# Optimization experiments

Hardware: AMD Instinct MI355X
Metric: run time of the kernel (lower is better)

Reference implementation:

```python
import jax, jax.numpy as jnp
import numpy as np
import math

H = 12          # num_attention_heads
DH = 64         # attention_head_size
D = H * DH      # hidden_size = 768
LN_EPS = 1e-5
GAUSS_W = 0.3989422804014327
WIDS = [None, 0.1, 1.0, 5.0]


def gauss_weight(L, wid):
    # faithful to generate_gauss_weight: row-normalized Gaussian bump per query pos
    center = (jnp.arange(L, dtype=jnp.float32) / L)[:, None]       # (L,1)
    pos = jnp.linspace(0.0, 1.0, L, dtype=jnp.float32)[None, :]    # (1,L)
    width = max(wid, 0.01) / 9.0                                   # static python scalar
    g = (GAUSS_W / width) * jnp.exp(-(pos - center) ** 2 / (2.0 * width * width))
    return g / jnp.max(g, axis=-1, keepdims=True)                  # (L,L)


def layer_norm(x, g, b):
    mu = jnp.mean(x, axis=-1, keepdims=True)
    var = jnp.mean((x - mu) ** 2, axis=-1, keepdims=True)
    return (x - mu) * jax.lax.rsqrt(var + LN_EPS) * g + b


def bert_attention(x, mask, qkv_w, qkv_b, out_w, out_b, ln_g, ln_b, wid):
    # x: (N,L,D); mask: (N,L,L); qkv_w: (3,D,D); qkv_b: (3,D)
    N, L, _ = x.shape

    def heads(t):  # (N,L,D) -> (N,H,L,DH)
        return t.reshape(N, L, H, DH).transpose(0, 2, 1, 3)

    q = heads(x @ qkv_w[0] + qkv_b[0])
    k = heads(x @ qkv_w[1] + qkv_b[1])
    v = heads(x @ qkv_w[2] + qkv_b[2])

    scores = jnp.einsum('nhqd,nhkd->nhqk', q, k) / math.sqrt(DH)   # (N,H,L,L)
    if wid is not None:
        scores = scores * gauss_weight(L, wid)[None, None]          # multiplicative GMM mask
    scores = scores + (1.0 - mask[:, None, :, :]) * -10000.0
    probs = jax.nn.softmax(scores, axis=-1)                         # dropout = identity (eval)
    ctx = jnp.einsum('nhqk,nhkd->nhqd', probs, v)                   # (N,H,L,DH)
    ctx = ctx.transpose(0, 2, 1, 3).reshape(N, L, D)

    proj = ctx @ out_w + out_b
    return layer_norm(proj + x, ln_g, ln_b)


def setup_inputs() -> dict:
    key = jax.random.key(0)
    ks = jax.random.split(key, 4)
    N, L = 4, 1024
    s = 0.02
    return {
        'input_tensor': jax.random.normal(ks[0], (N, L, D), dtype=jnp.float32),
        'attention_mask': jnp.ones((N, L, L), dtype=jnp.float32),
        'qkv_w': jax.random.normal(ks[1], (4, 3, D, D), dtype=jnp.float32) * s,
        'qkv_b': jnp.zeros((4, 3, D), dtype=jnp.float32),
        'out_w': jax.random.normal(ks[2], (4, D, D), dtype=jnp.float32) * s,
        'out_b': jnp.zeros((4, D), dtype=jnp.float32),
        'ln_g': jnp.ones((4, D), dtype=jnp.float32),
        'ln_b': jnp.zeros((4, D), dtype=jnp.float32),
    }


def reference(input_tensor, attention_mask, qkv_w, qkv_b, out_w, out_b, ln_g, ln_b):
    # pure_block=False path: 4 parallel GMM-masked attention branches, averaged
    outs = [
        bert_attention(input_tensor, attention_mask,
                       qkv_w[i], qkv_b[i], out_w[i], out_b[i], ln_g[i], ln_b[i], WIDS[i])
        for i in range(4)
    ]
    return jnp.mean(jnp.stack(outs, axis=-1), axis=-1)
```

## Files before the change

### kernel.cpp

```cpp
#include <hip/hip_runtime.h>
#include <hip/hip_bf16.h>

#define NB 4
#define LQ 1024
#define NH 12
#define DHD 64
#define DM 768
#define MTOT (NB*LQ)
#define L2E 1.4426950408889634f
#define SMB 11.541560327111708f
#define CFAR 3.3546262790251185e-4f

typedef __attribute__((ext_vector_type(4))) float f32x4;
typedef __attribute__((ext_vector_type(8))) short bf16x8;
typedef __attribute__((ext_vector_type(4))) short short4v;
typedef unsigned short u16;

#if __has_builtin(__builtin_amdgcn_exp2f)
#define EXP2(x) __builtin_amdgcn_exp2f(x)
#else
#define EXP2(x) __expf((x) * 0.6931471805599453f)
#endif

#define VMCNT(n) asm volatile("s_waitcnt vmcnt(" #n ")" ::: "memory")
#define RAW_BAR() __builtin_amdgcn_s_barrier()

__device__ __forceinline__ u16 f2bf(float f){
  union { float f; unsigned int i; } v; v.f = f;
  unsigned int r = v.i + 0x7FFFu + ((v.i >> 16) & 1u);
  return (u16)(r >> 16);
}
__device__ __forceinline__ float bf2f(u16 u){
  union { unsigned int i; float f; } v; v.i = ((unsigned int)u) << 16;
  return v.f;
}
__device__ __forceinline__ unsigned cvt_pk_bf16(float lo, float hi){
  unsigned r;
  asm("v_cvt_pk_bf16_f32 %0, %1, %2" : "=v"(r) : "v"(lo), "v"(hi));
  return r;
}

typedef const __attribute__((address_space(1))) void* gas_t;
typedef __attribute__((address_space(3))) void* las_t;
__device__ __forceinline__ void gload16(const void* g, void* l){
  __builtin_amdgcn_global_load_lds((gas_t)g, (las_t)l, 16, 0, 0);
}

__global__ void k_cvt_x(const float* __restrict__ x, u16* __restrict__ xb){
  int i = (blockIdx.x * 256 + threadIdx.x) * 4;
  float4 v = *reinterpret_cast<const float4*>(x + i);
  short4v o;
  o[0] = (short)f2bf(v.x); o[1] = (short)f2bf(v.y);
  o[2] = (short)f2bf(v.z); o[3] = (short)f2bf(v.w);
  *reinterpret_cast<short4v*>(xb + i) = o;
}

__global__ void k_wt(const float* __restrict__ qkv_w, const float* __restrict__ out_w,
                     u16* __restrict__ wt){
  int mat = blockIdx.z;
  const float* W = (mat < 12) ? (qkv_w + (size_t)mat*DM*DM)
                              : (out_w + (size_t)(mat-12)*DM*DM);
  __shared__ float tile[32][33];
  int j0 = blockIdx.x*32, k0 = blockIdx.y*32;
  int tx = threadIdx.x, ty = threadIdx.y;
  #pragma unroll
  for (int i=0;i<4;i++)
    tile[ty + i*8][tx] = W[(size_t)(k0 + ty + i*8)*DM + j0 + tx];
  __syncthreads();
  u16* dst = wt + (size_t)mat*DM*DM;
  int tid = ty*32 + tx;
  int jj = tid >> 3, kq = tid & 7;
  short4v pk;
  #pragma unroll
  for (int t=0;t<4;t++) pk[t] = (short)f2bf(tile[kq*4 + t][jj]);
  *reinterpret_cast<short4v*>(&dst[(size_t)(j0 + jj)*DM + k0 + kq*4]) = pk;
}

__global__ void k_maskchk(const float* __restrict__ mask, unsigned* __restrict__ flags){
  int qt = blockIdx.x, kt = blockIdx.y, n = blockIdx.z;
  const float* M = mask + ((size_t)(n*LQ) + qt*64)*LQ + kt*64;
  int tid = threadIdx.x;
  int r = tid >> 2, c4 = (tid & 3) * 16;
  int ok = 1;
  #pragma unroll
  for (int j=0;j<4;j++){
    float4 v = *reinterpret_cast<const float4*>(M + (size_t)r*LQ + c4 + j*4);
    ok &= (v.x==1.f) & (v.y==1.f) & (v.z==1.f) & (v.w==1.f);
  }
  __shared__ int sok[4];
  unsigned long long bal = __ballot(ok);
  if ((tid & 63) == 0) sok[tid>>6] = (bal == 0xFFFFFFFFFFFFFFFFull) ? 1 : 0;
  __syncthreads();
  if (tid == 0) flags[((size_t)n*16 + qt)*16 + kt] = sok[0] & sok[1] & sok[2] & sok[3];
}

__global__ __launch_bounds__(256) void k_vsum(const u16* __restrict__ qkvws, float* __restrict__ ps){
  const int nh = blockIdx.x;
  const int b  = blockIdx.y;
  const size_t blk = (size_t)NB*NH*LQ*DHD;
  const u16* Vt = qkvws + (size_t)(b*3+2)*blk + (size_t)nh*DHD*LQ;
  const int tid = threadIdx.x;
  const int dh = tid >> 2, c = tid & 3;
  float* psb = ps + ((size_t)(b*48 + nh)*17)*64;
  float acc = 0.f;
  for (int kt = 0; kt < 16; ++kt){
    if (c == 0) psb[kt*64 + dh] = acc;
    bf16x8 v0 = *reinterpret_cast<const bf16x8*>(&Vt[(size_t)dh*LQ + kt*64 + c*16]);
    bf16x8 v1 = *reinterpret_cast<const bf16x8*>(&Vt[(size_t)dh*LQ + kt*64 + c*16 + 8]);
    float s = 0.f;
    #pragma unroll
    for (int j=0;j<8;j++) s += bf2f((u16)v0[j]) + bf2f((u16)v1[j]);
    s += __shfl_xor(s, 1);
    s += __shfl_xor(s, 2);
    acc += s;
  }
  if (c == 0) psb[16*64 + dh] = acc;
}

__device__ __forceinline__ void gemm_tile32(const u16* __restrict__ Ag,
                                            const u16* __restrict__ Bg,
                                            u16* smem, f32x4 acc[4][4])
{
  const int tid = threadIdx.x, lane = tid & 63, w = tid >> 6;
  const int wr = (w >> 1) * 64, wc = (w & 1) * 64;
  const int rl = lane & 15, q4 = lane >> 4;
  const int srow = tid >> 2;
  const int su = (tid & 3) ^ ((srow >> 1) & 3);

  #define QSTG(buf, k0_) { \
    _Pragma("unroll") \
    for (int r = 0; r < 2; ++r){ \
      gload16(Ag + (size_t)(r*64 + srow)*DM + (k0_) + su*8, smem + (buf)*8192 + r*2048 + tid*8); \
      gload16(Bg + (size_t)(r*64 + srow)*DM + (k0_) + su*8, smem + (buf)*8192 + 4096 + r*2048 + tid*8); \
    } }

  QSTG(0, 0);
  QSTG(1, 32);
  int cur = 0, nxt2 = 2;
  for (int it = 0; it < 24; ++it){
    if (it + 2 < 24){
      QSTG(nxt2, (it+2)*32);
      VMCNT(8);
    } else if (it + 1 < 24){
      VMCNT(4);
    } else {
      VMCNT(0);
    }
    RAW_BAR();
    __builtin_amdgcn_sched_barrier(0);
    const u16* al = smem + cur*8192;
    const u16* bl = al + 4096;
    bf16x8 af[4], bfr[4];
    #pragma unroll
    for (int f = 0; f < 4; ++f){
      int ra = wr + f*16 + rl, rb = wc + f*16 + rl;
      int ua = q4 ^ ((ra >> 1) & 3), ub = q4 ^ ((rb >> 1) & 3);
      af[f]  = *reinterpret_cast<const bf16x8*>(&al[ra*32 + ua*8]);
      bfr[f] = *reinterpret_cast<const bf16x8*>(&bl[rb*32 + ub*8]);
    }
    #pragma unroll
    for (int mf=0; mf<4; ++mf)
      #pragma unroll
      for (int nf=0; nf<4; ++nf)
        acc[mf][nf] = __builtin_amdgcn_mfma_f32_16x16x32_bf16(af[mf], bfr[nf], acc[mf][nf], 0,0,0);
    RAW_BAR();
    cur = cur + 1 == 3 ? 0 : cur + 1;
    nxt2 = nxt2 + 1 == 3 ? 0 : nxt2 + 1;
  }
  #undef QSTG
}

__global__ __launch_bounds__(256) void k_qkv(const u16* __restrict__ xb, const u16* __restrict__ wt,
                     const float* __restrict__ qkv_b, u16* __restrict__ qkvws)
{
  __shared__ __align__(16) u16 smem[24576];
  const int bid = blockIdx.x;
  const int orig = (bid & 7) * 288 + (bid >> 3);
  const int j0 = (orig % 6) * 128;
  const int m0 = ((orig / 6) % 32) * 128;
  const int mat = orig / 192;
  const int t = mat % 3;
  f32x4 acc[4][4] = {};
  gemm_tile32(xb + (size_t)m0*DM, wt + (size_t)mat*DM*DM + (size_t)j0*DM, smem, acc);

  const int tid = threadIdx.x, lane = tid & 63, w = tid >> 6;
  const int wr = (w >> 1) * 64, wc = (w & 1) * 64;
  const int rl = lane & 15, rg = (lane >> 4) * 4;
  const float sc = (t == 0) ? 0.125f : 1.0f;
  const size_t matbase = (size_t)mat * ((size_t)NB*NH*LQ*DHD);
  if (t < 2){
    #pragma unroll
    for (int nf=0; nf<4; ++nf){
      int jc = wc + nf*16 + rl;
      float bias = qkv_b[mat*DM + j0 + jc];
      #pragma unroll
      for (int mf=0; mf<4; ++mf){
        int row = wr + mf*16 + rg;
        #pragma unroll
        for (int i=0;i<4;i++)
          smem[(row+i)*136 + jc] = f2bf((acc[mf][nf][i] + bias) * sc);
      }
    }
    __syncthreads();
    const int n = m0 >> 10, l0 = m0 & 1023;
    const int hbase = j0 >> 6;
    #pragma unroll
    for (int jj=0; jj<8; ++jj){
      int idx = tid + 256*jj;
      int l = idx >> 4, ch = idx & 15;
      bf16x8 v = *reinterpret_cast<const bf16x8*>(&smem[l*136 + ch*8]);
      int hh = hbase + (ch >> 3);
      int dh0 = (ch & 7) * 8;
      *reinterpret_cast<bf16x8*>(
        &qkvws[matbase + ((size_t)(n*NH + hh)*LQ + l0 + l)*DHD + dh0]) = v;
    }
  } else {
    #pragma unroll
    for (int nf=0; nf<4; ++nf){
      int j = j0 + wc + nf*16 + rl;
      float bias = qkv_b[mat*DM + j];
      int h = j >> 6, dh = j & 63;
      #pragma unroll
      for (int mf=0; mf<4; ++mf){
        int mB = m0 + wr + mf*16 + rg;
        int n = mB >> 10, l = mB & 1023;
        short4v pk;
        #pragma unroll
        for (int i=0;i<4;i++) pk[i] = (short)f2bf(acc[mf][nf][i] + bias);
        *reinterpret_cast<short4v*>(&qkvws[matbase + ((size_t)(n*NH + h)*DHD + dh)*LQ + l]) = pk;
      }
    }
  }
}

__global__ __launch_bounds__(512) void k_attn(const u16* __restrict__ qkvws, const float* __restrict__ mask,
                      const unsigned* __restrict__ flags, const float* __restrict__ ps,
                      u16* __restrict__ ctx, float c2_1, float c2_2, float c2_3)
{
  __shared__ __align__(16) u16 kv_lds[2][2][64*64];
  __shared__ __align__(16) u16 p_lds[128*64];
  const int bid = blockIdx.x;
  const int orig = (bid & 7) * 192 + (bid >> 3);
  const int qp = orig & 7;
  const int b  = (orig >> 3) & 3;
  const int nh = orig >> 5;
  const int n = nh / NH, h = nh % NH;
  const float c2 = (b==1) ? c2_1 : (b==2) ? c2_2 : c2_3;
  const bool useG = (b != 0);
  const int tid = threadIdx.x, lane = tid & 63, w = tid >> 6;
  const int wl = w & 3, half = w >> 2;
  const int qt = qp*2 + half;
  const int rl = lane & 15, q4 = lane >> 4, kc8 = q4*8, rg = q4*4;
  const int q0 = qt*64 + wl*16;

  const size_t hb = (size_t)(n*NH + h);
  const size_t blk = (size_t)NB*NH*LQ*DHD;
  const u16* Qb = qkvws + (size_t)(b*3+0)*blk + hb*LQ*DHD;
  const u16* Kb = qkvws + (size_t)(b*3+1)*blk + hb*LQ*DHD;
  const u16* Vt = qkvws + (size_t)(b*3+2)*blk + hb*DHD*LQ;
  const float* Mb = mask + (size_t)n*LQ*LQ;

  bf16x8 qf0 = *reinterpret_cast<const bf16x8*>(&Qb[(size_t)(q0+rl)*DHD + kc8]);
  bf16x8 qf1 = *reinterpret_cast<const bf16x8*>(&Qb[(size_t)(q0+rl)*DHD + 32 + kc8]);

  float srun[4] = {0.f,0.f,0.f,0.f};
  float dmin2[4], cq[4];
  f32x4 o[4] = {};
  #pragma unroll
  for (int i=0;i<4;i++){
    int q = q0 + rg + i;
    float c = (float)q * (1.0f/1024.0f);
    float ksf = floorf(c * 1023.0f + 0.5f);
    float dm = ksf * (1.0f/1023.0f) - c;
    cq[i] = c; dmin2[i] = dm*dm;
  }

  int lo_a, hi_a, lo_b, hi_b, ra_a, ra_b;
  {
    int qa = qp*2, qb = qp*2+1;
    int r0 = 1, r1 = 1;
    for (int t = 0; t < 16; ++t){
      r0 &= (flags[((size_t)n*16 + qa)*16 + t] != 0u) ? 1 : 0;
      r1 &= (flags[((size_t)n*16 + qb)*16 + t] != 0u) ? 1 : 0;
    }
    ra_a = r0; ra_b = r1;
    lo_a = 0; hi_a = 16; lo_b = 0; hi_b = 16;
    if (r0){
      if (b == 1){ lo_a = qa>0?qa-1:0; hi_a = qa<15?qa+2:16; }
      else if (b == 2){ lo_a = qa>5?qa-5:0; hi_a = qa<10?qa+6:16; }
    }
    if (r1){
      if (b == 1){ lo_b = qb>0?qb-1:0; hi_b = qb<15?qb+2:16; }
      else if (b == 2){ lo_b = qb>5?qb-5:0; hi_b = qb<10?qb+6:16; }
    }
  }
  const int mylo = half ? lo_b : lo_a;
  const int myhi = half ? hi_b : hi_a;
  const int myrowall = half ? ra_b : ra_a;
  const int blo = lo_a < lo_b ? lo_a : lo_b;
  const int bhi = hi_a > hi_b ? hi_a : hi_b;
  const int mynt = myhi - mylo;

  if (myrowall && mynt < 16){
    const float* psb = ps + ((size_t)(b*48 + nh)*17)*64;
    #pragma unroll
    for (int nf=0; nf<4; ++nf){
      int dh = nf*16 + rl;
      float sfar = psb[16*64 + dh] - psb[myhi*64 + dh] + psb[mylo*64 + dh];
      float fv = CFAR * sfar;
      #pragma unroll
      for (int i=0;i<4;i++) o[nf][i] = fv;
    }
    float sinit = CFAR * (float)(64*(16 - mynt));
    #pragma unroll
    for (int i=0;i<4;i++) srun[i] = sinit;
  }

  const int r8 = tid >> 3;
  const int uu = (tid & 7) ^ (r8 & 7);

  #define STAGE8(buf, kt_) { \
    gload16(Kb + (size_t)((kt_)*64 + r8)*DHD + uu*8, (u16*)kv_lds[buf][0] + tid*8); \
    gload16(Vt + (size_t)r8*LQ + (kt_)*64 + uu*8, (u16*)kv_lds[buf][1] + tid*8); }

  STAGE8(0, blo);

  const int nloop = bhi - blo;
  for (int it = 0; it < nloop; ++it){
    const int kt = blo + it;
    const int cur = it & 1;
    if (it + 1 < nloop){
      STAGE8(cur^1, kt+1);
      VMCNT(2);
    } else {
      VMCNT(0);
    }
    RAW_BAR();
    __builtin_amdgcn_sched_barrier(0);

    if (kt >= mylo && kt < myhi){
      const bool allones = myrowall || (flags[((size_t)n*16 + qt)*16 + kt] != 0u);
      const u16* kbuf = (const u16*)kv_lds[cur][0];
      const u16* vbuf = (const u16*)kv_lds[cur][1];

      f32x4 sf[4] = {};
      __builtin_amdgcn_s_setprio(1);
      #pragma unroll
      for (int nf=0; nf<4; ++nf){
        int row = nf*16 + rl, sw = (row & 7) << 3;
        bf16x8 kf0 = *reinterpret_cast<const bf16x8*>(&kbuf[row*64 + (kc8 ^ sw)]);
        bf16x8 kf1 = *reinterpret_cast<const bf16x8*>(&kbuf[row*64 + ((32 + kc8) ^ sw)]);
        sf[nf] = __builtin_amdgcn_mfma_f32_16x16x32_bf16(qf0, kf0, sf[nf], 0,0,0);
        sf[nf] = __builtin_amdgcn_mfma_f32_16x16x32_bf16(qf1, kf1, sf[nf], 0,0,0);
      }
      __builtin_amdgcn_s_setprio(0);

      float pv[4][4];
      #pragma unroll
      for (int nf=0; nf<4; ++nf){
        int key = kt*64 + nf*16 + rl;
        float pos = (float)key * (1.0f/1023.0f);
        #pragma unroll
        for (int i=0;i<4;i++){
          float s = sf[nf][i];
          if (useG){
            float d = pos - cq[i];
            float tg = fmaf(-d, d, dmin2[i]);
            s *= EXP2(tg * c2);
          }
          if (!allones){
            int q = q0 + rg + i;
            s = fmaf(1.0f - Mb[(size_t)q*LQ + key], -10000.0f, s);
          }
          float p = EXP2(fmaf(s, L2E, -SMB));
          srun[i] += p;
          pv[nf][i] = p;
        }
      }

      #pragma unroll
      for (int np=0; np<2; ++np)
        #pragma unroll
        for (int i=0;i<4;i++){
          unsigned u = cvt_pk_bf16(pv[np*2][i], pv[np*2+1][i]);
          int row = w*16 + rg + i, sw = (row & 7) << 3;
          p_lds[row*64 + ((np*32 + rl) ^ sw)]      = (u16)(u & 0xffffu);
          p_lds[row*64 + ((np*32 + 16 + rl) ^ sw)] = (u16)(u >> 16);
        }
      asm volatile("s_waitcnt lgkmcnt(0)" ::: "memory");
      __builtin_amdgcn_sched_barrier(0);

      {
        int prow = w*16 + rl, psw = (prow & 7) << 3;
        bf16x8 pa0 = *reinterpret_cast<const bf16x8*>(&p_lds[prow*64 + (kc8 ^ psw)]);
        bf16x8 pa1 = *reinterpret_cast<const bf16x8*>(&p_lds[prow*64 + ((32 + kc8) ^ psw)]);
        __builtin_amdgcn_s_setprio(1);
        #pragma unroll
        for (int nf=0; nf<4; ++nf){
          int row = nf*16 + rl, sw = (row & 7) << 3;
          bf16x8 vv0 = *reinterpret_cast<const bf16x8*>(&vbuf[row*64 + (kc8 ^ sw)]);
          bf16x8 vv1 = *reinterpret_cast<const bf16x8*>(&vbuf[row*64 + ((32 + kc8) ^ sw)]);
          o[nf] = __builtin_amdgcn_mfma_f32_16x16x32_bf16(pa0, vv0, o[nf], 0,0,0);
          o[nf] = __builtin_amdgcn_mfma_f32_16x16x32_bf16(pa1, vv1, o[nf], 0,0,0);
        }
        __builtin_amdgcn_s_setprio(0);
      }
    }
    RAW_BAR();
  }

  #pragma unroll
  for (int off=1; off<16; off<<=1){
    #pragma unroll
    for (int i=0;i<4;i++) srun[i] += __shfl_xor(srun[i], off);
  }
  #pragma unroll
  for (int i=0;i<4;i++){
    float inv = 1.0f / (srun[i] + 1e-35f);
    int q = q0 + rg + i;
    size_t mrow = ((size_t)(n*LQ + q)) * DM;
    #pragma unroll
    for (int nf=0; nf<4; ++nf){
      int d = h*DHD + nf*16 + rl;
      ctx[(size_t)b*((size_t)MTOT*DM) + mrow + d] = f2bf(o[nf][i] * inv);
    }
  }
  #undef STAGE8
}

__global__ __launch_bounds__(256) void k_proj(const u16* __restrict__ ctx, const u16* __restrict__ wt,
                      const float* __restrict__ out_b, u16* __restrict__ proj)
{
  __shared__ __align__(16) u16 smem[24576];
  const int bid = blockIdx.x;
  const int orig = (bid & 7) * 96 + (bid >> 3);
  const int j0 = (orig % 6) * 128;
  const int m0 = ((orig / 6) % 32) * 128;
  const int b = orig / 192;
  f32x4 acc[4][4] = {};
  gemm_tile32(ctx + (size_t)b*MTOT*DM + (size_t)m0*DM,
              wt + (size_t)(12+b)*DM*DM + (size_t)j0*DM, smem, acc);
  const int tid = threadIdx.x, lane = tid & 63, w = tid >> 6;
  const int wr = (w >> 1) * 64, wc = (w & 1) * 64;
  const int rl = lane & 15, rg = (lane >> 4) * 4;
  #pragma unroll
  for (int nf=0; nf<4; ++nf){
    int jc = wc + nf*16 + rl;
    float bias = out_b[b*DM + j0 + jc];
    #pragma unroll
    for (int mf=0; mf<4; ++mf){
      int row = wr + mf*16 + rg;
      #pragma unroll
      for (int i=0;i<4;i++)
        smem[(row+i)*136 + jc] = f2bf(acc[mf][nf][i] + bias);
    }
  }
  __syncthreads();
  #pragma unroll
  for (int jj=0; jj<8; ++jj){
    int idx = tid + 256*jj;
    int l = idx >> 4, ch = idx & 15;
    bf16x8 v = *reinterpret_cast<const bf16x8*>(&smem[l*136 + ch*8]);
    *reinterpret_cast<bf16x8*>(&proj[((size_t)b*MTOT + m0 + l)*DM + j0 + ch*8]) = v;
  }
}

__global__ __launch_bounds__(256) void k_ln(const float* __restrict__ x, const u16* __restrict__ proj,
                    const float* __restrict__ ln_g, const float* __restrict__ ln_b,
                    float* __restrict__ out)
{
  const int m = blockIdx.x;
  const int tid = threadIdx.x, lane = tid & 63, w = tid >> 6;
  __shared__ float rb[4][2][4];
  float xr[3], acc[3] = {0.f,0.f,0.f};
  #pragma unroll
  for (int c=0;c<3;c++) xr[c] = x[(size_t)m*DM + tid + c*256];
  float vv[4][3], s1[4], s2[4];
  #pragma unroll
  for (int b=0;b<4;b++){
    s1[b] = 0.f; s2[b] = 0.f;
    #pragma unroll
    for (int c=0;c<3;c++){
      float v = bf2f(proj[((size_t)b*MTOT + m)*DM + tid + c*256]) + xr[c];
      vv[b][c] = v; s1[b] += v; s2[b] += v*v;
    }
  }
  #pragma unroll
  for (int b=0;b<4;b++){
    #pragma unroll
    for (int off=32; off>=1; off>>=1){
      s1[b] += __shfl_xor(s1[b], off);
      s2[b] += __shfl_xor(s2[b], off);
    }
    if (lane == 0){ rb[b][0][w] = s1[b]; rb[b][1][w] = s2[b]; }
  }
  __syncthreads();
  #pragma unroll
  for (int b=0;b<4;b++){
    float S1 = rb[b][0][0]+rb[b][0][1]+rb[b][0][2]+rb[b][0][3];
    float S2 = rb[b][1][0]+rb[b][1][1]+rb[b][1][2]+rb[b][1][3];
    float mu = S1 * (1.0f/768.0f);
    float var = S2 * (1.0f/768.0f) - mu*mu;
    float rs = rsqrtf(var + 1e-5f);
    #pragma unroll
    for (int c=0;c<3;c++){
      int j = tid + c*256;
      acc[c] += 0.25f * ((vv[b][c]-mu)*rs*ln_g[b*DM+j] + ln_b[b*DM+j]);
    }
  }
  #pragma unroll
  for (int c=0;c<3;c++) out[(size_t)m*DM + tid + c*256] = acc[c];
}

extern "C" void kernel_launch(void* const* d_in, const int* in_sizes, int n_in,
                              void* d_out, int out_size, void* d_ws, size_t ws_size,
                              hipStream_t stream)
{
  const float* x     = (const float*)d_in[0];
  const float* mask  = (const float*)d_in[1];
  const float* qkv_w = (const float*)d_in[2];
  const float* qkv_b = (const float*)d_in[3];
  const float* out_w = (const float*)d_in[4];
  const float* out_b = (const float*)d_in[5];
  const float* ln_g  = (const float*)d_in[6];
  const float* ln_b  = (const float*)d_in[7];
  float* out = (float*)d_out;
  char* ws = (char*)d_ws;

  u16* xb        = (u16*)(ws);
  unsigned* flags= (unsigned*)(ws);
  float* ps      = (float*)(ws + 8192);
  u16* wt        = (u16*)(ws + 6291456);
  u16* qkv       = (u16*)(ws + 25165824);
  u16* ctx       = (u16*)(ws + 100663296);
  u16* proj      = (u16*)(ws + 25165824);

  float c2[3];
  const float wid[3] = {0.1f, 1.0f, 5.0f};
  for (int i=0;i<3;i++){
    float wdt = wid[i]/9.0f;
    c2[i] = (1.0f/(2.0f*wdt*wdt)) * L2E;
  }

  k_cvt_x<<<dim3(3072), dim3(256), 0, stream>>>(x, xb);
  k_wt<<<dim3(24,24,16), dim3(32,8), 0, stream>>>(qkv_w, out_w, wt);
  k_qkv<<<dim3(2304), dim3(256), 0, stream>>>(xb, wt, qkv_b, qkv);
  k_vsum<<<dim3(48,4), dim3(256), 0, stream>>>(qkv, ps);
  k_maskchk<<<dim3(16,16,4), dim3(256), 0, stream>>>(mask, flags);
  k_attn<<<dim3(1536), dim3(512), 0, stream>>>(qkv, mask, flags, ps, ctx, c2[0], c2[1], c2[2]);
  k_proj<<<dim3(768), dim3(256), 0, stream>>>(ctx, wt, out_b, proj);
  k_ln<<<dim3(4096), dim3(256), 0, stream>>>(x, proj, ln_g, ln_b, out);
}
```

Baseline: 240.1 us.

## Merge narrow-window attention branches into one block to balance work

Changes the attention grid from one block per (branch, head, query-pair) to three job types. One block runs branch 0 (full) plus branch 1 (narrow band), and the other two branches each get their own block, for 1152 blocks instead of 1536. The aim is to even out per-block work, since branch 1 touches only about 3 key tiles when the mask is all ones, and to cut block launch overhead. The cost is a longer serial chain in the merged blocks and a second Q load and setup inside the lambda.

```diff
diff --git a/kernel.cpp b/kernel.cpp
--- a/kernel.cpp
+++ b/kernel.cpp
@@ -240,32 +240,22 @@
   __shared__ __align__(16) u16 kv_lds[2][2][64*64];
   __shared__ __align__(16) u16 p_lds[128*64];
   const int bid = blockIdx.x;
-  const int orig = (bid & 7) * 192 + (bid >> 3);
+  const int orig = (bid & 7) * 144 + (bid >> 3);
   const int qp = orig & 7;
-  const int b  = (orig >> 3) & 3;
-  const int nh = orig >> 5;
+  const int r  = orig >> 3;
+  const int jb = r % 3;
+  const int nh = r / 3;
   const int n = nh / NH, h = nh % NH;
-  const float c2 = (b==1) ? c2_1 : (b==2) ? c2_2 : c2_3;
-  const bool useG = (b != 0);
   const int tid = threadIdx.x, lane = tid & 63, w = tid >> 6;
   const int wl = w & 3, half = w >> 2;
   const int qt = qp*2 + half;
   const int rl = lane & 15, q4 = lane >> 4, kc8 = q4*8, rg = q4*4;
   const int q0 = qt*64 + wl*16;
 
-  const size_t hb = (size_t)(n*NH + h);
   const size_t blk = (size_t)NB*NH*LQ*DHD;
-  const u16* Qb = qkvws + (size_t)(b*3+0)*blk + hb*LQ*DHD;
-  const u16* Kb = qkvws + (size_t)(b*3+1)*blk + hb*LQ*DHD;
-  const u16* Vt = qkvws + (size_t)(b*3+2)*blk + hb*DHD*LQ;
   const float* Mb = mask + (size_t)n*LQ*LQ;
 
-  bf16x8 qf0 = *reinterpret_cast<const bf16x8*>(&Qb[(size_t)(q0+rl)*DHD + kc8]);
-  bf16x8 qf1 = *reinterpret_cast<const bf16x8*>(&Qb[(size_t)(q0+rl)*DHD + 32 + kc8]);
-
-  float srun[4] = {0.f,0.f,0.f,0.f};
   float dmin2[4], cq[4];
-  f32x4 o[4] = {};
   #pragma unroll
   for (int i=0;i<4;i++){
     int q = q0 + rg + i;
@@ -275,157 +265,176 @@
     cq[i] = c; dmin2[i] = dm*dm;
   }
 
-  int lo_a, hi_a, lo_b, hi_b, ra_a, ra_b;
+  int ra_a = 1, ra_b = 1;
   {
     int qa = qp*2, qb = qp*2+1;
-    int r0 = 1, r1 = 1;
     for (int t = 0; t < 16; ++t){
-      r0 &= (flags[((size_t)n*16 + qa)*16 + t] != 0u) ? 1 : 0;
-      r1 &= (flags[((size_t)n*16 + qb)*16 + t] != 0u) ? 1 : 0;
-    }
-    ra_a = r0; ra_b = r1;
-    lo_a = 0; hi_a = 16; lo_b = 0; hi_b = 16;
-    if (r0){
-      if (b == 1){ lo_a = qa>0?qa-1:0; hi_a = qa<15?qa+2:16; }
-      else if (b == 2){ lo_a = qa>5?qa-5:0; hi_a = qa<10?qa+6:16; }
-    }
-    if (r1){
-      if (b == 1){ lo_b = qb>0?qb-1:0; hi_b = qb<15?qb+2:16; }
-      else if (b == 2){ lo_b = qb>5?qb-5:0; hi_b = qb<10?qb+6:16; }
-    }
-  }
-  const int mylo = half ? lo_b : lo_a;
-  const int myhi = half ? hi_b : hi_a;
+      ra_a &= (flags[((size_t)n*16 + qa)*16 + t] != 0u) ? 1 : 0;
+      ra_b &= (flags[((size_t)n*16 + qb)*16 + t] != 0u) ? 1 : 0;
+    }
+  }
   const int myrowall = half ? ra_b : ra_a;
-  const int blo = lo_a < lo_b ? lo_a : lo_b;
-  const int bhi = hi_a > hi_b ? hi_a : hi_b;
-  const int mynt = myhi - mylo;
-
-  if (myrowall && mynt < 16){
-    const float* psb = ps + ((size_t)(b*48 + nh)*17)*64;
-    #pragma unroll
-    for (int nf=0; nf<4; ++nf){
-      int dh = nf*16 + rl;
-      float sfar = psb[16*64 + dh] - psb[myhi*64 + dh] + psb[mylo*64 + dh];
-      float fv = CFAR * sfar;
-      #pragma unroll
-      for (int i=0;i<4;i++) o[nf][i] = fv;
-    }
-    float sinit = CFAR * (float)(64*(16 - mynt));
-    #pragma unroll
-    for (int i=0;i<4;i++) srun[i] = sinit;
-  }
 
   const int r8 = tid >> 3;
   const int uu = (tid & 7) ^ (r8 & 7);
 
-  #define STAGE8(buf, kt_) { \
-    gload16(Kb + (size_t)((kt_)*64 + r8)*DHD + uu*8, (u16*)kv_lds[buf][0] + tid*8); \
-    gload16(Vt + (size_t)r8*LQ + (kt_)*64 + uu*8, (u16*)kv_lds[buf][1] + tid*8); }
-
-  STAGE8(0, blo);
-
-  const int nloop = bhi - blo;
-  for (int it = 0; it < nloop; ++it){
-    const int kt = blo + it;
-    const int cur = it & 1;
-    if (it + 1 < nloop){
-      STAGE8(cur^1, kt+1);
-      VMCNT(2);
-    } else {
-      VMCNT(0);
-    }
-    RAW_BAR();
-    __builtin_amdgcn_sched_barrier(0);
-
-    if (kt >= mylo && kt < myhi){
-      const bool allones = myrowall || (flags[((size_t)n*16 + qt)*16 + kt] != 0u);
-      const u16* kbuf = (const u16*)kv_lds[cur][0];
-      const u16* vbuf = (const u16*)kv_lds[cur][1];
-
-      f32x4 sf[4] = {};
-      __builtin_amdgcn_s_setprio(1);
+  auto pass = [&](const int b, const float c2){
+    const bool useG = (b != 0);
+    const u16* Qb = qkvws + (size_t)(b*3+0)*blk + (size_t)nh*LQ*DHD;
+    const u16* Kb = qkvws + (size_t)(b*3+1)*blk + (size_t)nh*LQ*DHD;
+    const u16* Vt = qkvws + (size_t)(b*3+2)*blk + (size_t)nh*DHD*LQ;
+
+    bf16x8 qf0 = *reinterpret_cast<const bf16x8*>(&Qb[(size_t)(q0+rl)*DHD + kc8]);
+    bf16x8 qf1 = *reinterpret_cast<const bf16x8*>(&Qb[(size_t)(q0+rl)*DHD + 32 + kc8]);
+
+    float srun[4] = {0.f,0.f,0.f,0.f};
+    f32x4 o[4] = {};
+
+    int lo_a = 0, hi_a = 16, lo_b2 = 0, hi_b2 = 16;
+    {
+      int qa = qp*2, qb = qp*2+1;
+      if (ra_a){
+        if (b == 1){ lo_a = qa>0?qa-1:0; hi_a = qa<15?qa+2:16; }
+        else if (b == 2){ lo_a = qa>5?qa-5:0; hi_a = qa<10?qa+6:16; }
+      }
+      if (ra_b){
+        if (b == 1){ lo_b2 = qb>0?qb-1:0; hi_b2 = qb<15?qb+2:16; }
+        else if (b == 2){ lo_b2 = qb>5?qb-5:0; hi_b2 = qb<10?qb+6:16; }
+      }
+    }
+    const int mylo = half ? lo_b2 : lo_a;
+    const int myhi = half ? hi_b2 : hi_a;
+    const int blo = lo_a < lo_b2 ? lo_a : lo_b2;
+    const int bhi = hi_a > hi_b2 ? hi_a : hi_b2;
+    const int mynt = myhi - mylo;
+
+    if (myrowall && mynt < 16){
+      const float* psb = ps + ((size_t)(b*48 + nh)*17)*64;
       #pragma unroll
       for (int nf=0; nf<4; ++nf){
-        int row = nf*16 + rl, sw = (row & 7) << 3;
-        bf16x8 kf0 = *reinterpret_cast<const bf16x8*>(&kbuf[row*64 + (kc8 ^ sw)]);
-        bf16x8 kf1 = *reinterpret_cast<const bf16x8*>(&kbuf[row*64 + ((32 + kc8) ^ sw)]);
-        sf[nf] = __builtin_amdgcn_mfma_f32_16x16x32_bf16(qf0, kf0, sf[nf], 0,0,0);
-        sf[nf] = __builtin_amdgcn_mfma_f32_16x16x32_bf16(qf1, kf1, sf[nf], 0,0,0);
-      }
-      __builtin_amdgcn_s_setprio(0);
-
-      float pv[4][4];
-      #pragma unroll
-      for (int nf=0; nf<4; ++nf){
-        int key = kt*64 + nf*16 + rl;
-        float pos = (float)key * (1.0f/1023.0f);
+        int dh = nf*16 + rl;
+        float sfar = psb[16*64 + dh] - psb[myhi*64 + dh] + psb[mylo*64 + dh];
+        float fv = CFAR * sfar;
         #pragma unroll
-        for (int i=0;i<4;i++){
-          float s = sf[nf][i];
-          if (useG){
-            float d = pos - cq[i];
-            float tg = fmaf(-d, d, dmin2[i]);
-            s *= EXP2(tg * c2);
-          }
-          if (!allones){
-            int q = q0 + rg + i;
-            s = fmaf(1.0f - Mb[(size_t)q*LQ + key], -10000.0f, s);
-          }
-          float p = EXP2(fmaf(s, L2E, -SMB));
-          srun[i] += p;
-          pv[nf][i] = p;
-        }
-      }
-
-      #pragma unroll
-      for (int np=0; np<2; ++np)
-        #pragma unroll
-        for (int i=0;i<4;i++){
-          unsigned u = cvt_pk_bf16(pv[np*2][i], pv[np*2+1][i]);
-          int row = w*16 + rg + i, sw = (row & 7) << 3;
-          p_lds[row*64 + ((np*32 + rl) ^ sw)]      = (u16)(u & 0xffffu);
-          p_lds[row*64 + ((np*32 + 16 + rl) ^ sw)] = (u16)(u >> 16);
-        }
-      asm volatile("s_waitcnt lgkmcnt(0)" ::: "memory");
+        for (int i=0;i<4;i++) o[nf][i] = fv;
+      }
+      float sinit = CFAR * (float)(64*(16 - mynt));
+      #pragma unroll
+      for (int i=0;i<4;i++) srun[i] = sinit;
+    }
+
+    #define STAGE8(buf, kt_) { \
+      gload16(Kb + (size_t)((kt_)*64 + r8)*DHD + uu*8, (u16*)kv_lds[buf][0] + tid*8); \
+      gload16(Vt + (size_t)r8*LQ + (kt_)*64 + uu*8, (u16*)kv_lds[buf][1] + tid*8); }
+
+    STAGE8(0, blo);
+
+    const int nloop = bhi - blo;
+    for (int it = 0; it < nloop; ++it){
+      const int kt = blo + it;
+      const int cur = it & 1;
+      if (it + 1 < nloop){
+        STAGE8(cur^1, kt+1);
+        VMCNT(2);
+      } else {
+        VMCNT(0);
+      }
+      RAW_BAR();
       __builtin_amdgcn_sched_barrier(0);
 
-      {
-        int prow = w*16 + rl, psw = (prow & 7) << 3;
-        bf16x8 pa0 = *reinterpret_cast<const bf16x8*>(&p_lds[prow*64 + (kc8 ^ psw)]);
-        bf16x8 pa1 = *reinterpret_cast<const bf16x8*>(&p_lds[prow*64 + ((32 + kc8) ^ psw)]);
+      if (kt >= mylo && kt < myhi){
+        const bool allones = myrowall || (flags[((size_t)n*16 + qt)*16 + kt] != 0u);
+        const u16* kbuf = (const u16*)kv_lds[cur][0];
+        const u16* vbuf = (const u16*)kv_lds[cur][1];
+
+        f32x4 sf[4] = {};
         __builtin_amdgcn_s_setprio(1);
         #pragma unroll
         for (int nf=0; nf<4; ++nf){
           int row = nf*16 + rl, sw = (row & 7) << 3;
-          bf16x8 vv0 = *reinterpret_cast<const bf16x8*>(&vbuf[row*64 + (kc8 ^ sw)]);
-          bf16x8 vv1 = *reinterpret_cast<const bf16x8*>(&vbuf[row*64 + ((32 + kc8) ^ sw)]);
-          o[nf] = __builtin_amdgcn_mfma_f32_16x16x32_bf16(pa0, vv0, o[nf], 0,0,0);
-          o[nf] = __builtin_amdgcn_mfma_f32_16x16x32_bf16(pa1, vv1, o[nf], 0,0,0);
+          bf16x8 kf0 = *reinterpret_cast<const bf16x8*>(&kbuf[row*64 + (kc8 ^ sw)]);
+          bf16x8 kf1 = *reinterpret_cast<const bf16x8*>(&kbuf[row*64 + ((32 + kc8) ^ sw)]);
+          sf[nf] = __builtin_amdgcn_mfma_f32_16x16x32_bf16(qf0, kf0, sf[nf], 0,0,0);
+          sf[nf] = __builtin_amdgcn_mfma_f32_16x16x32_bf16(qf1, kf1, sf[nf], 0,0,0);
         }
         __builtin_amdgcn_s_setprio(0);
-      }
-    }
-    RAW_BAR();
-  }
-
-  #pragma unroll
-  for (int off=1; off<16; off<<=1){
-    #pragma unroll
-    for (int i=0;i<4;i++) srun[i] += __shfl_xor(srun[i], off);
-  }
-  #pragma unroll
-  for (int i=0;i<4;i++){
-    float inv = 1.0f / (srun[i] + 1e-35f);
-    int q = q0 + rg + i;
-    size_t mrow = ((size_t)(n*LQ + q)) * DM;
-    #pragma unroll
-    for (int nf=0; nf<4; ++nf){
-      int d = h*DHD + nf*16 + rl;
-      ctx[(size_t)b*((size_t)MTOT*DM) + mrow + d] = f2bf(o[nf][i] * inv);
-    }
-  }
-  #undef STAGE8
+
+        float pv[4][4];
+        #pragma unroll
+        for (int nf=0; nf<4; ++nf){
+          int key = kt*64 + nf*16 + rl;
+          float pos = (float)key * (1.0f/1023.0f);
+          #pragma unroll
+          for (int i=0;i<4;i++){
+            float s = sf[nf][i];
+            if (useG){
+              float d = pos - cq[i];
+              float tg = fmaf(-d, d, dmin2[i]);
+              s *= EXP2(tg * c2);
+            }
+            if (!allones){
+              int q = q0 + rg + i;
+              s = fmaf(1.0f - Mb[(size_t)q*LQ + key], -10000.0f, s);
+            }
+            float p = EXP2(fmaf(s, L2E, -SMB));
+            srun[i] += p;
+            pv[nf][i] = p;
+          }
+        }
+
+        #pragma unroll
+        for (int np=0; np<2; ++np)
+          #pragma unroll
+          for (int i=0;i<4;i++){
+            unsigned u = cvt_pk_bf16(pv[np*2][i], pv[np*2+1][i]);
+            int row = w*16 + rg + i, sw = (row & 7) << 3;
+            p_lds[row*64 + ((np*32 + rl) ^ sw)]      = (u16)(u & 0xffffu);
+            p_lds[row*64 + ((np*32 + 16 + rl) ^ sw)] = (u16)(u >> 16);
+          }
+        asm volatile("s_waitcnt lgkmcnt(0)" ::: "memory");
+        __builtin_amdgcn_sched_barrier(0);
+
+        {
+          int prow = w*16 + rl, psw = (prow & 7) << 3;
+          bf16x8 pa0 = *reinterpret_cast<const bf16x8*>(&p_lds[prow*64 + (kc8 ^ psw)]);
+          bf16x8 pa1 = *reinterpret_cast<const bf16x8*>(&p_lds[prow*64 + ((32 + kc8) ^ psw)]);
+          __builtin_amdgcn_s_setprio(1);
+          #pragma unroll
+          for (int nf=0; nf<4; ++nf){
+            int row = nf*16 + rl, sw = (row & 7) << 3;
+            bf16x8 vv0 = *reinterpret_cast<const bf16x8*>(&vbuf[row*64 + (kc8 ^ sw)]);
+            bf16x8 vv1 = *reinterpret_cast<const bf16x8*>(&vbuf[row*64 + ((32 + kc8) ^ sw)]);
+            o[nf] = __builtin_amdgcn_mfma_f32_16x16x32_bf16(pa0, vv0, o[nf], 0,0,0);
+            o[nf] = __builtin_amdgcn_mfma_f32_16x16x32_bf16(pa1, vv1, o[nf], 0,0,0);
+          }
+          __builtin_amdgcn_s_setprio(0);
+        }
+      }
+      RAW_BAR();
+    }
+    #undef STAGE8
+
+    #pragma unroll
+    for (int off=1; off<16; off<<=1){
+      #pragma unroll
+      for (int i=0;i<4;i++) srun[i] += __shfl_xor(srun[i], off);
+    }
+    #pragma unroll
+    for (int i=0;i<4;i++){
+      float inv = 1.0f / (srun[i] + 1e-35f);
+      int q = q0 + rg + i;
+      size_t mrow = ((size_t)(n*LQ + q)) * DM;
+      #pragma unroll
+      for (int nf=0; nf<4; ++nf){
+        int d = h*DHD + nf*16 + rl;
+        ctx[(size_t)b*((size_t)MTOT*DM) + mrow + d] = f2bf(o[nf][i] * inv);
+      }
+    }
+  };
+
+  if (jb == 0){ pass(0, 0.f); pass(1, c2_1); }
+  else if (jb == 1){ pass(2, c2_2); }
+  else { pass(3, c2_3); }
 }
 
 __global__ __launch_bounds__(256) void k_proj(const u16* __restrict__ ctx, const u16* __restrict__ wt,
@@ -547,7 +556,7 @@
   k_qkv<<<dim3(2304), dim3(256), 0, stream>>>(xb, wt, qkv_b, qkv);
   k_vsum<<<dim3(48,4), dim3(256), 0, stream>>>(qkv, ps);
   k_maskchk<<<dim3(16,16,4), dim3(256), 0, stream>>>(mask, flags);
-  k_attn<<<dim3(1536), dim3(512), 0, stream>>>(qkv, mask, flags, ps, ctx, c2[0], c2[1], c2[2]);
+  k_attn<<<dim3(1152), dim3(512), 0, stream>>>(qkv, mask, flags, ps, ctx, c2[0], c2[1], c2[2]);
   k_proj<<<dim3(768), dim3(256), 0, stream>>>(ctx, wt, out_b, proj);
   k_ln<<<dim3(4096), dim3(256), 0, stream>>>(x, proj, ln_g, ln_b, out);
 }
```

Measured after the change: 231.8 us, median of 2. 1.04x faster.
